# Kernel optimization log

Hardware: AMD Instinct MI355X
Metric: run time of the kernel (lower is better)

Reference implementation:

```python
import jax, jax.numpy as jnp
import numpy as np
import math

EMBED_DIM = 1024
NUM_HEADS = 16
HEAD_DIM = EMBED_DIM // NUM_HEADS
DIFFUSION_STEPS = 2
ALPHA = 0.05
DETACH_P = True


def setup_inputs() -> dict:
    key = jax.random.key(0)
    ks = jax.random.split(key, 9)
    B, N, D = 1, 2048, EMBED_DIM
    s = 1.0 / math.sqrt(D)
    inp = {
        "hidden_states": jax.random.normal(ks[0], (B, N, D), dtype=jnp.float32),
        # torch nn.Linear weight is [out,in]; we store [in,out] so y = x @ W + b
        "Wq": jax.random.normal(ks[1], (D, D), dtype=jnp.float32) * s,
        "bq": jnp.zeros((D,), dtype=jnp.float32),
        "Wk": jax.random.normal(ks[2], (D, D), dtype=jnp.float32) * s,
        "bk": jnp.zeros((D,), dtype=jnp.float32),
        "Wv": jax.random.normal(ks[3], (D, D), dtype=jnp.float32) * s,
        "bv": jnp.zeros((D,), dtype=jnp.float32),
        "Wo": jax.random.normal(ks[4], (D, D), dtype=jnp.float32) * s,
        "bo": jnp.zeros((D,), dtype=jnp.float32),
    }
    return inp


def reference(hidden_states, Wq, bq, Wk, bk, Wv, bv, Wo, bo):
    B, N, D = hidden_states.shape
    H, hd = NUM_HEADS, HEAD_DIM

    def split_heads(x):  # [B,N,D] -> [B,H,N,hd]
        return x.reshape(B, N, H, hd).transpose(0, 2, 1, 3)

    Q = split_heads(hidden_states @ Wq + bq)
    K = split_heads(hidden_states @ Wk + bk)
    V = split_heads(hidden_states @ Wv + bv)

    # standard QK^T attention probabilities
    scores = jnp.einsum('bhqd,bhkd->bhqk', Q, K) / math.sqrt(hd)
    p0 = jax.nn.softmax(scores, axis=-1)

    # transition matrix from keys (note: scaled by sqrt(embed_dim), not head_dim)
    sim = jnp.einsum('bhid,bhjd->bhij', K, K) / math.sqrt(D)
    P = jax.nn.softmax(sim, axis=-1)
    if DETACH_P:
        P = jax.lax.stop_gradient(P)

    # iterative diffusion: p <- (1-alpha)*p0 + alpha * p @ P
    p = p0
    for _ in range(DIFFUSION_STEPS):
        p = (1.0 - ALPHA) * p0 + ALPHA * jnp.einsum('bhqn,bhnm->bhqm', p, P)

    attn = jnp.einsum('bhqk,bhkd->bhqd', p, V)          # [B,H,N,hd]
    attn = attn.transpose(0, 2, 1, 3).reshape(B, N, H * hd)
    out = attn @ Wo + bo
    return out, p
```

## Files before the change

### kernel.cpp

```cpp
#include <hip/hip_runtime.h>

#define N_TOK 2048
#define DMODEL 1024
#define NHEAD 16
#define HDIM 64

typedef __attribute__((ext_vector_type(8))) __bf16 bf16x8;
typedef __attribute__((ext_vector_type(4))) float f32x4;
typedef __attribute__((ext_vector_type(4))) int i32x4;
typedef __attribute__((ext_vector_type(8))) int i32x8;

__device__ __forceinline__ float bf2f(unsigned short h) {
  return __uint_as_float(((unsigned int)h) << 16);
}
__device__ __forceinline__ unsigned short f2bf(float f) {
  unsigned int u = __float_as_uint(f);
  unsigned int r = (u + 0x7fffu + ((u >> 16) & 1u)) >> 16;
  return (unsigned short)r;
}
__device__ __forceinline__ unsigned int pack4_fp8(float a, float b, float c, float d) {
  int v = __builtin_amdgcn_cvt_pk_fp8_f32(a, b, 0, false);
  v = __builtin_amdgcn_cvt_pk_fp8_f32(c, d, v, true);
  return (unsigned int)v;
}
__device__ __forceinline__ int swz8(int k8, int row) {
  return k8 ^ ((row & 7) << 4);
}

__device__ __forceinline__ void async16(const void* g, void* l) {
  __builtin_amdgcn_global_load_lds((__attribute__((address_space(1))) void*)(g),
                                   (__attribute__((address_space(3))) void*)(l),
                                   16, 0, 0);
}

#define FP8_SCALE 256.0f
#define FP8_INV2  (1.0f / (256.0f * 256.0f))

struct GemmP {
  const unsigned short* A;
  const unsigned short* B;
  const unsigned short* Eb;
  const float* bias;
  float* Cf;
  unsigned short* Cb;
  long long sA, sB, sE, sCf, sCb;
  int lda, ldb, ldE, ldCf, ldCb;
  int M, N, K;
  float alpha, beta;
};

__global__ __launch_bounds__(256) void gemm_bt_kernel(GemmP g) {
  __shared__ __attribute__((aligned(16))) unsigned short As[128 * 32];
  __shared__ __attribute__((aligned(16))) unsigned short Bs[128 * 32];
  const int tid = threadIdx.x;
  const int lane = tid & 63;
  const int wv = tid >> 6;
  const int wr = wv >> 1, wc = wv & 1;
  const long long z = blockIdx.z;
  const unsigned short* A = g.A + z * g.sA;
  const unsigned short* B = g.B + z * g.sB;
  const int tm = blockIdx.y * 128;
  const int tn = blockIdx.x * 128;

  const int r0 = tid >> 2;
  const int r1 = (tid + 256) >> 2;
  const int kof = (tid & 3) * 8;
  int bn0 = tn + r0; if (bn0 > g.N - 1) bn0 = g.N - 1;
  int bn1 = tn + r1; if (bn1 > g.N - 1) bn1 = g.N - 1;

  const unsigned short* pa0 = A + (long long)(tm + r0) * g.lda + kof;
  const unsigned short* pa1 = A + (long long)(tm + r1) * g.lda + kof;
  const unsigned short* pb0 = B + (long long)bn0 * g.ldb + kof;
  const unsigned short* pb1 = B + (long long)bn1 * g.ldb + kof;

  unsigned short* la0 = &As[tid * 8];
  unsigned short* la1 = &As[(tid + 256) * 8];
  unsigned short* lb0 = &Bs[tid * 8];
  unsigned short* lb1 = &Bs[(tid + 256) * 8];

  const int aroff = (wr * 64 + (lane & 15)) * 32 + (lane >> 4) * 8;
  const int broff = (wc * 64 + (lane & 15)) * 32 + (lane >> 4) * 8;

  f32x4 acc[4][4] = {};

  for (int kk = 0; kk < g.K; kk += 32) {
    __syncthreads();
    async16(pa0 + kk, la0);
    async16(pa1 + kk, la1);
    async16(pb0 + kk, lb0);
    async16(pb1 + kk, lb1);
    __syncthreads();
    bf16x8 af[4], bfr[4];
#pragma unroll
    for (int i = 0; i < 4; i++)
      af[i] = *(const bf16x8*)&As[aroff + i * 16 * 32];
#pragma unroll
    for (int j = 0; j < 4; j++)
      bfr[j] = *(const bf16x8*)&Bs[broff + j * 16 * 32];
#pragma unroll
    for (int i = 0; i < 4; i++)
#pragma unroll
      for (int j = 0; j < 4; j++)
        acc[i][j] = __builtin_amdgcn_mfma_f32_16x16x32_bf16(af[i], bfr[j], acc[i][j], 0, 0, 0);
  }

  const unsigned short* Eb = g.Eb ? g.Eb + z * g.sE : nullptr;
  float* Cf = g.Cf ? g.Cf + z * g.sCf : nullptr;
  unsigned short* Cb = g.Cb ? g.Cb + z * g.sCb : nullptr;
  const int cbase = tn + wc * 64 + (lane & 15);
  const int rbase = tm + wr * 64 + (lane >> 4) * 4;
#pragma unroll
  for (int i = 0; i < 4; i++) {
#pragma unroll
    for (int j = 0; j < 4; j++) {
      int col = cbase + j * 16;
      if (col < g.N) {
        float bs = g.bias ? g.bias[col] : 0.f;
#pragma unroll
        for (int r = 0; r < 4; r++) {
          int row = rbase + i * 16 + r;
          float v = g.alpha * acc[i][j][r] + bs;
          if (Eb) v += g.beta * bf2f(Eb[(long long)row * g.ldE + col]);
          if (Cf) Cf[(long long)row * g.ldCf + col] = v;
          if (Cb) Cb[(long long)row * g.ldCb + col] = f2bf(v);
        }
      }
    }
  }
}

struct QKP {
  const unsigned short* A;
  const unsigned short* B;
  float* mx;
  float* rz;
  unsigned short* Pbf;
  unsigned char* P8;
  float scale;
  int colstats;
};

__global__ __launch_bounds__(256) void qk_stats_kernel(QKP g) {
  __shared__ __attribute__((aligned(16))) unsigned short Qs[128 * 64];
  __shared__ __attribute__((aligned(16))) unsigned short Ks[2][128 * 64];
  __shared__ float redA[2][128];
  __shared__ float redB[2][128];
  const int tid = threadIdx.x;
  const int lane = tid & 63;
  const int wv = tid >> 6;
  const int wr = wv >> 1, wc = wv & 1;
  const int z = blockIdx.y;
  const int tm = blockIdx.x * 128;
  const unsigned short* A = g.A + z * HDIM;
  const unsigned short* B = g.B + z * HDIM;

  int sr[4], so[4];
#pragma unroll
  for (int k = 0; k < 4; k++) {
    int c = tid + k * 256;
    int row = c >> 3;
    sr[k] = row;
    so[k] = ((c & 7) ^ (row & 7)) * 8;
  }
#pragma unroll
  for (int k = 0; k < 4; k++)
    async16(A + (long long)(tm + sr[k]) * DMODEL + so[k], (char*)Qs + tid * 16 + k * 4096);
#pragma unroll
  for (int k = 0; k < 4; k++)
    async16(B + (long long)sr[k] * DMODEL + so[k], (char*)Ks[0] + tid * 16 + k * 4096);
  asm volatile("s_waitcnt vmcnt(0)" ::: "memory");
  __builtin_amdgcn_s_barrier();

  const int fr = lane & 15;
  const int fg = lane >> 4;
  bf16x8 qf[4][2];
#pragma unroll
  for (int i = 0; i < 4; i++)
#pragma unroll
    for (int s = 0; s < 2; s++) {
      int r = wr * 64 + fr + i * 16;
      int gl = (fg + s * 4) ^ (r & 7);
      qf[i][s] = *(const bf16x8*)&Qs[r * 64 + gl * 8];
    }

  float m_[16], s_[16], mn_[16], t_[16];
#pragma unroll
  for (int q = 0; q < 16; q++) { m_[q] = -3.0e38f; s_[q] = 0.f; }

  int buf = 0;
  for (int kb = 0; kb < 16; kb++) {
    f32x4 acc[4][4] = {};
#pragma unroll
    for (int j = 0; j < 4; j++) {
      int r = wc * 64 + fr + j * 16;
#pragma unroll
      for (int s = 0; s < 2; s++) {
        int gl = (fg + s * 4) ^ (r & 7);
        bf16x8 bf = *(const bf16x8*)&Ks[buf][r * 64 + gl * 8];
#pragma unroll
        for (int i = 0; i < 4; i++)
          acc[i][j] = __builtin_amdgcn_mfma_f32_16x16x32_bf16(qf[i][s], bf, acc[i][j], 0, 0, 0);
      }
    }
    if (kb < 15) {
#pragma unroll
      for (int k = 0; k < 4; k++)
        async16(B + (long long)((kb + 1) * 128 + sr[k]) * DMODEL + so[k],
                (char*)Ks[buf ^ 1] + tid * 16 + k * 4096);
    }
#pragma unroll
    for (int i = 0; i < 4; i++)
#pragma unroll
      for (int r = 0; r < 4; r++) {
        float mm = fmaxf(fmaxf(acc[i][0][r], acc[i][1][r]),
                         fmaxf(acc[i][2][r], acc[i][3][r]));
        mn_[i * 4 + r] = mm * g.scale;
      }
#pragma unroll
    for (int q = 0; q < 16; q++) {
      float v = mn_[q];
      v = fmaxf(v, __shfl_xor(v, 1));
      v = fmaxf(v, __shfl_xor(v, 2));
      v = fmaxf(v, __shfl_xor(v, 4));
      v = fmaxf(v, __shfl_xor(v, 8));
      mn_[q] = v;
    }
    if (fr == 0) {
#pragma unroll
      for (int i = 0; i < 4; i++)
#pragma unroll
        for (int r = 0; r < 4; r++)
          redA[wc][wr * 64 + i * 16 + fg * 4 + r] = mn_[i * 4 + r];
    }
    __builtin_amdgcn_s_barrier();
#pragma unroll
    for (int i = 0; i < 4; i++)
#pragma unroll
      for (int r = 0; r < 4; r++) {
        int row = wr * 64 + i * 16 + fg * 4 + r;
        int q = i * 4 + r;
        float mn = fmaxf(m_[q], fmaxf(redA[0][row], redA[1][row]));
        float e0 = __expf(acc[i][0][r] * g.scale - mn);
        float e1 = __expf(acc[i][1][r] * g.scale - mn);
        float e2 = __expf(acc[i][2][r] * g.scale - mn);
        float e3 = __expf(acc[i][3][r] * g.scale - mn);
        t_[q] = (e0 + e1) + (e2 + e3);
        mn_[q] = mn;
      }
#pragma unroll
    for (int q = 0; q < 16; q++) {
      float v = t_[q];
      v += __shfl_xor(v, 1);
      v += __shfl_xor(v, 2);
      v += __shfl_xor(v, 4);
      v += __shfl_xor(v, 8);
      t_[q] = v;
    }
    if (fr == 0) {
#pragma unroll
      for (int i = 0; i < 4; i++)
#pragma unroll
        for (int r = 0; r < 4; r++)
          redB[wc][wr * 64 + i * 16 + fg * 4 + r] = t_[i * 4 + r];
    }
    __builtin_amdgcn_s_barrier();
#pragma unroll
    for (int i = 0; i < 4; i++)
#pragma unroll
      for (int r = 0; r < 4; r++) {
        int row = wr * 64 + i * 16 + fg * 4 + r;
        int q = i * 4 + r;
        float tt = redB[0][row] + redB[1][row];
        s_[q] = s_[q] * __expf(m_[q] - mn_[q]) + tt;
        m_[q] = mn_[q];
      }
    if (kb < 15) asm volatile("s_waitcnt vmcnt(0)" ::: "memory");
    __builtin_amdgcn_s_barrier();
    buf ^= 1;
  }

  if (fr == 0 && wc == 0) {
#pragma unroll
    for (int i = 0; i < 4; i++)
#pragma unroll
      for (int r = 0; r < 4; r++) {
        int row = wr * 64 + i * 16 + fg * 4 + r;
        int q = i * 4 + r;
        g.mx[(long long)z * N_TOK + tm + row] = m_[q];
        g.rz[(long long)z * N_TOK + tm + row] = 1.f / s_[q];
      }
  }
}

__global__ __launch_bounds__(256) void qk_emit_kernel(QKP g) {
  __shared__ __attribute__((aligned(16))) unsigned short Qs[128 * 64];
  __shared__ __attribute__((aligned(16))) unsigned short Ks[2][128 * 64];
  __shared__ __attribute__((aligned(16))) float Ps[128 * 128];
  const int tid = threadIdx.x;
  const int lane = tid & 63;
  const int wv = tid >> 6;
  const int wr = wv >> 1, wc = wv & 1;
  const int z = blockIdx.y;
  const int tm = blockIdx.x * 128;
  const unsigned short* A = g.A + z * HDIM;
  const unsigned short* B = g.B + z * HDIM;

  int sr[4], so[4];
#pragma unroll
  for (int k = 0; k < 4; k++) {
    int c = tid + k * 256;
    int row = c >> 3;
    sr[k] = row;
    so[k] = ((c & 7) ^ (row & 7)) * 8;
  }
#pragma unroll
  for (int k = 0; k < 4; k++)
    async16(A + (long long)(tm + sr[k]) * DMODEL + so[k], (char*)Qs + tid * 16 + k * 4096);
#pragma unroll
  for (int k = 0; k < 4; k++)
    async16(B + (long long)sr[k] * DMODEL + so[k], (char*)Ks[0] + tid * 16 + k * 4096);
  asm volatile("s_waitcnt vmcnt(0)" ::: "memory");
  __builtin_amdgcn_s_barrier();

  const int fr = lane & 15;
  const int fg = lane >> 4;
  bf16x8 qf[4][2];
#pragma unroll
  for (int i = 0; i < 4; i++)
#pragma unroll
    for (int s = 0; s < 2; s++) {
      int r = wr * 64 + fr + i * 16;
      int gl = (fg + s * 4) ^ (r & 7);
      qf[i][s] = *(const bf16x8*)&Qs[r * 64 + gl * 8];
    }

  const int rr = tid >> 5;
  const int c4 = (tid & 31) * 4;
  const long long zn = (long long)z * N_TOK;
  float mr_[16], rr_[16];
  if (!g.colstats) {
#pragma unroll
    for (int p = 0; p < 16; p++) {
      mr_[p] = g.mx[zn + tm + p * 8 + rr];
      rr_[p] = g.rz[zn + tm + p * 8 + rr];
    }
  }

  int buf = 0;
  for (int kb = 0; kb < 16; kb++) {
    f32x4 acc[4][4] = {};
#pragma unroll
    for (int j = 0; j < 4; j++) {
      int r = wc * 64 + fr + j * 16;
#pragma unroll
      for (int s = 0; s < 2; s++) {
        int gl = (fg + s * 4) ^ (r & 7);
        bf16x8 bf = *(const bf16x8*)&Ks[buf][r * 64 + gl * 8];
#pragma unroll
        for (int i = 0; i < 4; i++)
          acc[i][j] = __builtin_amdgcn_mfma_f32_16x16x32_bf16(qf[i][s], bf, acc[i][j], 0, 0, 0);
      }
    }
#pragma unroll
    for (int i = 0; i < 4; i++)
#pragma unroll
      for (int j = 0; j < 4; j++)
#pragma unroll
        for (int r = 0; r < 4; r++)
          Ps[(wr * 64 + i * 16 + fg * 4 + r) * 128 + wc * 64 + fr + j * 16] =
              acc[i][j][r] * g.scale;
    __builtin_amdgcn_s_barrier();
    if (kb < 15) {
#pragma unroll
      for (int k = 0; k < 4; k++)
        async16(B + (long long)((kb + 1) * 128 + sr[k]) * DMODEL + so[k],
                (char*)Ks[buf ^ 1] + tid * 16 + k * 4096);
    }
    const int ct = kb * 128;
    float ma[4], ra[4];
    if (g.colstats) {
      float4 m4 = *(const float4*)&g.mx[zn + ct + c4];
      float4 r4 = *(const float4*)&g.rz[zn + ct + c4];
      ma[0] = m4.x; ma[1] = m4.y; ma[2] = m4.z; ma[3] = m4.w;
      ra[0] = r4.x; ra[1] = r4.y; ra[2] = r4.z; ra[3] = r4.w;
    }
#pragma unroll
    for (int p = 0; p < 16; p++) {
      int row = p * 8 + rr;
      f32x4 v = *(const f32x4*)&Ps[row * 128 + c4];
      float pr[4];
      if (g.colstats) {
        pr[0] = __expf(v.x - ma[0]) * ra[0];
        pr[1] = __expf(v.y - ma[1]) * ra[1];
        pr[2] = __expf(v.z - ma[2]) * ra[2];
        pr[3] = __expf(v.w - ma[3]) * ra[3];
      } else {
        pr[0] = __expf(v.x - mr_[p]) * rr_[p];
        pr[1] = __expf(v.y - mr_[p]) * rr_[p];
        pr[2] = __expf(v.z - mr_[p]) * rr_[p];
        pr[3] = __expf(v.w - mr_[p]) * rr_[p];
      }
      long long prow = (zn + tm + row) * N_TOK;
      if (g.Pbf) {
        uint2 ob;
        ob.x = (unsigned)f2bf(pr[0]) | ((unsigned)f2bf(pr[1]) << 16);
        ob.y = (unsigned)f2bf(pr[2]) | ((unsigned)f2bf(pr[3]) << 16);
        *(uint2*)&g.Pbf[prow + ct + c4] = ob;
      }
      unsigned o8 = pack4_fp8(pr[0] * FP8_SCALE, pr[1] * FP8_SCALE,
                              pr[2] * FP8_SCALE, pr[3] * FP8_SCALE);
      *(unsigned*)&g.P8[prow + ((ct + c4) ^ ((row & 7) << 4))] = o8;
    }
    if (kb < 15) asm volatile("s_waitcnt vmcnt(0)" ::: "memory");
    __builtin_amdgcn_s_barrier();
    buf ^= 1;
  }
}

struct Gemm8P {
  const unsigned char* A;
  const unsigned char* B;
  const unsigned short* Eb;
  float* Cf;
  unsigned short* Cb;
  long long sA, sB, sE, sCf, sCb;
  int lda, ldb, ldE, ldCf, ldCb;
  int K;
  float alpha, beta;
};

__global__ __launch_bounds__(256) void gemm_fp8_kernel(Gemm8P g) {
  __shared__ __attribute__((aligned(16))) unsigned char smem[65536];
  unsigned char* As0 = smem;
  unsigned char* Bs0 = smem + 32768;
  float* Cs = (float*)smem;
  const int tid = threadIdx.x;
  const int lane = tid & 63;
  const int wv = tid >> 6;
  const int wr = wv >> 1, wc = wv & 1;

  const unsigned int nx = gridDim.x, ny = gridDim.y;
  unsigned int orig = (blockIdx.z * ny + blockIdx.y) * nx + blockIdx.x;
  unsigned int nwg = nx * ny * gridDim.z;
  unsigned int wg = (orig & 7) * (nwg >> 3) + (orig >> 3);
  const int bx = wg % nx;
  unsigned int t1 = wg / nx;
  const int by = t1 % ny;
  const int bz = t1 / ny;

  const long long z = bz;
  const unsigned char* A = g.A + z * g.sA;
  const unsigned char* B = g.B + z * g.sB;
  const int tm = by * 128;
  const int tn = bx * 128;

  const int rs = tid >> 3;
  const int ks = (tid & 7) * 16;
  const unsigned char* pa0 = A + (long long)(tm + rs) * g.lda + ks;
  const unsigned char* pb0 = B + (long long)(tn + rs) * g.ldb + ks;
  const long long sa32 = 32LL * g.lda;
  const long long sb32 = 32LL * g.ldb;

  const int sw = (lane & 7) << 4;
  const int kg = (lane >> 4) * 32;
  const int klo = kg ^ sw;
  const int khi = (kg + 16) ^ sw;
  const int aoff0 = (wr * 64 + (lane & 15)) * 128;
  const int boff0 = (wc * 64 + (lane & 15)) * 128;

  f32x4 acc[4][4] = {};

  auto STAGE = [&](int buf, int kk) {
    unsigned char* la = As0 + buf * 16384 + tid * 16;
    unsigned char* lb = Bs0 + buf * 16384 + tid * 16;
    async16(pa0 + kk, la);
    async16(pa0 + sa32 + kk, la + 4096);
    async16(pa0 + 2 * sa32 + kk, la + 8192);
    async16(pa0 + 3 * sa32 + kk, la + 12288);
    async16(pb0 + kk, lb);
    async16(pb0 + sb32 + kk, lb + 4096);
    async16(pb0 + 2 * sb32 + kk, lb + 8192);
    async16(pb0 + 3 * sb32 + kk, lb + 12288);
  };

  auto COMPUTE = [&](int buf) {
    const unsigned char* ab = As0 + buf * 16384;
    const unsigned char* bb = Bs0 + buf * 16384;
    i32x8 a8[4], b8[4];
#pragma unroll
    for (int i = 0; i < 4; i++) {
      i32x4 lo = *(const i32x4*)(ab + aoff0 + i * 16 * 128 + klo);
      i32x4 hi = *(const i32x4*)(ab + aoff0 + i * 16 * 128 + khi);
      a8[i] = __builtin_shufflevector(lo, hi, 0, 1, 2, 3, 4, 5, 6, 7);
    }
#pragma unroll
    for (int j = 0; j < 4; j++) {
      i32x4 lo = *(const i32x4*)(bb + boff0 + j * 16 * 128 + klo);
      i32x4 hi = *(const i32x4*)(bb + boff0 + j * 16 * 128 + khi);
      b8[j] = __builtin_shufflevector(lo, hi, 0, 1, 2, 3, 4, 5, 6, 7);
    }
#pragma unroll
    for (int i = 0; i < 4; i++)
#pragma unroll
      for (int j = 0; j < 4; j++)
        acc[i][j] = __builtin_amdgcn_mfma_scale_f32_16x16x128_f8f6f4(
            a8[i], b8[j], acc[i][j], 0, 0, 0, 0x7f7f7f7f, 0, 0x7f7f7f7f);
  };

  const int NT = g.K >> 7;
  STAGE(0, 0);
  int cur = 0;
  for (int t = 0; t < NT - 1; ++t) {
    STAGE(cur ^ 1, (t + 1) << 7);
    asm volatile("s_waitcnt vmcnt(8)" ::: "memory");
    __builtin_amdgcn_s_barrier();
    __builtin_amdgcn_sched_barrier(0);
    COMPUTE(cur);
    __builtin_amdgcn_sched_barrier(0);
    __builtin_amdgcn_s_barrier();
    cur ^= 1;
  }
  asm volatile("s_waitcnt vmcnt(0)" ::: "memory");
  __builtin_amdgcn_s_barrier();
  __builtin_amdgcn_sched_barrier(0);
  COMPUTE(cur);

  __syncthreads();
  const int lrow0 = wr * 64 + (lane >> 4) * 4;
  const int lcol0 = wc * 64 + (lane & 15);
#pragma unroll
  for (int i = 0; i < 4; i++)
#pragma unroll
    for (int j = 0; j < 4; j++)
#pragma unroll
      for (int r = 0; r < 4; r++)
        Cs[(lrow0 + i * 16 + r) * 128 + lcol0 + j * 16] = acc[i][j][r];
  __syncthreads();

  const unsigned short* Eb = g.Eb + z * g.sE;
  float* Cf = g.Cf + z * g.sCf;
  unsigned short* Cb = g.Cb + z * g.sCb;
  const int rr = tid >> 5;
  const int c4 = (tid & 31) * 4;
#pragma unroll
  for (int p = 0; p < 16; p++) {
    int row = p * 8 + rr;
    f32x4 v = *(const f32x4*)&Cs[row * 128 + c4];
    long long gr = (long long)(tm + row);
    uint2 e = *(const uint2*)&Eb[gr * g.ldE + tn + c4];
    f32x4 o;
    o.x = g.alpha * v.x + g.beta * bf2f((unsigned short)(e.x & 0xffff));
    o.y = g.alpha * v.y + g.beta * bf2f((unsigned short)(e.x >> 16));
    o.z = g.alpha * v.z + g.beta * bf2f((unsigned short)(e.y & 0xffff));
    o.w = g.alpha * v.w + g.beta * bf2f((unsigned short)(e.y >> 16));
    *(f32x4*)&Cf[gr * g.ldCf + tn + c4] = o;
    uint2 ob;
    ob.x = (unsigned)f2bf(o.x) | ((unsigned)f2bf(o.y) << 16);
    ob.y = (unsigned)f2bf(o.z) | ((unsigned)f2bf(o.w) << 16);
    *(uint2*)&Cb[gr * g.ldCb + tn + c4] = ob;
  }
}

struct AttnP {
  const unsigned short* A;
  const unsigned short* B;
  float* Part;
  long long sA, sB;
  int lda, ldb, G;
};

__global__ __launch_bounds__(256) void attn_part_kernel(AttnP g) {
  __shared__ __attribute__((aligned(16))) unsigned short As[128 * 32];
  __shared__ __attribute__((aligned(16))) unsigned short Bs[64 * 32];
  const int tid = threadIdx.x;
  const int lane = tid & 63;
  const int w = tid >> 6;
  const int z = blockIdx.y;
  const int kz = blockIdx.z;
  const unsigned short* A = g.A + (long long)z * g.sA;
  const unsigned short* B = g.B + (long long)z * g.sB;
  const int tm = blockIdx.x * 128;
  const int k0 = kz * 512;

  const int rA0 = tid >> 2;
  const int rA1 = 64 + (tid >> 2);
  const int kof = (tid & 3) * 8;
  const unsigned short* pa0 = A + (long long)(tm + rA0) * g.lda + k0 + kof;
  const unsigned short* pa1 = A + (long long)(tm + rA1) * g.lda + k0 + kof;
  const unsigned short* pb0 = B + (long long)(tid >> 2) * g.ldb + k0 + kof;
  unsigned short* la0 = &As[tid * 8];
  unsigned short* la1 = &As[(tid + 256) * 8];
  unsigned short* lb0 = &Bs[tid * 8];

  const int aoff = (w * 32 + (lane & 15)) * 32 + (lane >> 4) * 8;
  const int boff = (lane & 15) * 32 + (lane >> 4) * 8;

  f32x4 acc[2][4] = {};

  for (int kk = 0; kk < 512; kk += 32) {
    __syncthreads();
    async16(pa0 + kk, la0);
    async16(pa1 + kk, la1);
    async16(pb0 + kk, lb0);
    __syncthreads();
    bf16x8 af[2], bfr[4];
#pragma unroll
    for (int i = 0; i < 2; i++)
      af[i] = *(const bf16x8*)&As[aoff + i * 16 * 32];
#pragma unroll
    for (int j = 0; j < 4; j++)
      bfr[j] = *(const bf16x8*)&Bs[boff + j * 16 * 32];
#pragma unroll
    for (int i = 0; i < 2; i++)
#pragma unroll
      for (int j = 0; j < 4; j++)
        acc[i][j] = __builtin_amdgcn_mfma_f32_16x16x32_bf16(af[i], bfr[j], acc[i][j], 0, 0, 0);
  }

  float* P = g.Part + ((long long)(kz * g.G + z) * N_TOK + tm) * 64;
#pragma unroll
  for (int i = 0; i < 2; i++) {
#pragma unroll
    for (int j = 0; j < 4; j++) {
      int col = (lane & 15) + j * 16;
#pragma unroll
      for (int r = 0; r < 4; r++) {
        int row = w * 32 + i * 16 + (lane >> 4) * 4 + r;
        P[(long long)row * 64 + col] = acc[i][j][r];
      }
    }
  }
}

__global__ __launch_bounds__(256) void attn_reduce_kernel(const float* Part, unsigned short* ATT,
                                                          int G, int h0) {
  int idx = blockIdx.x * 256 + threadIdx.x;
  int f = idx * 4;
  int z = f / (N_TOK * 64);
  int rem = f % (N_TOK * 64);
  int row = rem >> 6;
  int col = rem & 63;
  long long stride = (long long)G * N_TOK * 64;
  const float* p0 = Part + ((long long)z * N_TOK + row) * 64 + col;
  float4 s = *(const float4*)p0;
  float4 a = *(const float4*)(p0 + stride);
  float4 b = *(const float4*)(p0 + 2 * stride);
  float4 c = *(const float4*)(p0 + 3 * stride);
  s.x += a.x + b.x + c.x; s.y += a.y + b.y + c.y;
  s.z += a.z + b.z + c.z; s.w += a.w + b.w + c.w;
  uint2 o;
  o.x = (unsigned)f2bf(s.x) | ((unsigned)f2bf(s.y) << 16);
  o.y = (unsigned)f2bf(s.z) | ((unsigned)f2bf(s.w) << 16);
  *(uint2*)&ATT[(long long)row * DMODEL + (h0 + z) * 64 + col] = o;
}


__global__ __launch_bounds__(256) void cast_f32_bf16_kernel(const float* x, unsigned short* y) {
  int i = blockIdx.x * 256 + threadIdx.x;
  const float4* src = (const float4*)x;
  float4 a = src[i * 2], b = src[i * 2 + 1];
  uint4 o;
  o.x = (unsigned)f2bf(a.x) | ((unsigned)f2bf(a.y) << 16);
  o.y = (unsigned)f2bf(a.z) | ((unsigned)f2bf(a.w) << 16);
  o.z = (unsigned)f2bf(b.x) | ((unsigned)f2bf(b.y) << 16);
  o.w = (unsigned)f2bf(b.z) | ((unsigned)f2bf(b.w) << 16);
  ((uint4*)y)[i] = o;
}

__global__ __launch_bounds__(256) void transpose_w_kernel(const float* in, unsigned short* out,
                                                          int rows, int cols) {
  __shared__ float t[32][33];
  int c = blockIdx.x * 32 + threadIdx.x;
  int r0 = blockIdx.y * 32;
#pragma unroll
  for (int j = 0; j < 32; j += 8)
    t[threadIdx.y + j][threadIdx.x] = in[(long long)(r0 + threadIdx.y + j) * cols + c];
  __syncthreads();
  int r = r0 + threadIdx.x;
#pragma unroll
  for (int j = 0; j < 32; j += 8)
    out[(long long)(blockIdx.x * 32 + threadIdx.y + j) * rows + r] =
        f2bf(t[threadIdx.x][threadIdx.y + j]);
}

__global__ __launch_bounds__(256) void transpose_bf_kernel(const unsigned short* in,
                                                           unsigned short* out,
                                                           int rows, int cols) {
  __shared__ unsigned short t[32][34];
  int c = blockIdx.x * 32 + threadIdx.x;
  int r0 = blockIdx.y * 32;
#pragma unroll
  for (int j = 0; j < 32; j += 8)
    t[threadIdx.y + j][threadIdx.x] = in[(long long)(r0 + threadIdx.y + j) * cols + c];
  __syncthreads();
  int r = r0 + threadIdx.x;
#pragma unroll
  for (int j = 0; j < 32; j += 8)
    out[(long long)(blockIdx.x * 32 + threadIdx.y + j) * rows + r] = t[threadIdx.x][threadIdx.y + j];
}


extern "C" void kernel_launch(void* const* d_in, const int* in_sizes, int n_in,
                              void* d_out, int out_size, void* d_ws, size_t ws_size,
                              hipStream_t stream) {
  const float* hs = (const float*)d_in[0];
  const float* Wq = (const float*)d_in[1];
  const float* bq = (const float*)d_in[2];
  const float* Wk = (const float*)d_in[3];
  const float* bk = (const float*)d_in[4];
  const float* Wv = (const float*)d_in[5];
  const float* bv = (const float*)d_in[6];
  const float* Wo = (const float*)d_in[7];
  const float* bo = (const float*)d_in[8];
  float* out = (float*)d_out;
  float* outp = out + (size_t)N_TOK * DMODEL;

  char* base = (char*)d_ws;
  size_t off = 0;
  auto alloc = [&](size_t bytes) -> void* {
    void* p = base + off;
    off += (bytes + 255) & ~(size_t)255;
    return p;
  };
  const size_t ND2 = (size_t)N_TOK * DMODEL * 2;
  unsigned short* Xbf = (unsigned short*)alloc(ND2);
  unsigned short* Qbf = (unsigned short*)alloc(ND2);
  unsigned short* Kbf = (unsigned short*)alloc(ND2);
  unsigned short* Vbf = (unsigned short*)alloc(ND2);
  unsigned short* Vt  = (unsigned short*)alloc(ND2);
  unsigned short* ATT = (unsigned short*)alloc(ND2);
  unsigned short* WT  = (unsigned short*)alloc((size_t)DMODEL * DMODEL * 2);
  float* mx = (float*)alloc((size_t)NHEAD * N_TOK * 4);
  float* rz = (float*)alloc((size_t)NHEAD * N_TOK * 4);
  float* mxq = (float*)alloc((size_t)NHEAD * N_TOK * 4);
  float* rzq = (float*)alloc((size_t)NHEAD * N_TOK * 4);
  float* Part = (float*)alloc((size_t)4 * NHEAD * N_TOK * 64 * 4);
  size_t fixed = off;

  const size_t SZ = (size_t)N_TOK * N_TOK;
  int G = 16;
  while (G > 1 && fixed + (size_t)G * SZ * 8 > ws_size) G >>= 1;
  float* SB           = (float*)alloc((size_t)G * SZ * 4);
  unsigned short* P0  = (unsigned short*)alloc((size_t)G * SZ * 2);
  unsigned char* P0q  = (unsigned char*)alloc((size_t)G * SZ);
  unsigned char* PT   = (unsigned char*)alloc((size_t)G * SZ);
  unsigned short* PB   = (unsigned short*)SB + G * SZ;

  auto gemm = [&](const GemmP& p, int nt, int mt, int batch) {
    gemm_bt_kernel<<<dim3(nt, mt, batch), 256, 0, stream>>>(p);
  };

  cast_f32_bf16_kernel<<<(N_TOK * DMODEL / 8) / 256, 256, 0, stream>>>(hs, Xbf);

  auto proj = [&](const float* W, const float* bias, unsigned short* dst) {
    transpose_w_kernel<<<dim3(32, 32), dim3(32, 8), 0, stream>>>(W, WT, DMODEL, DMODEL);
    GemmP p = {};
    p.A = Xbf; p.lda = DMODEL;
    p.B = WT;  p.ldb = DMODEL;
    p.bias = bias;
    p.Cb = dst; p.ldCb = DMODEL;
    p.M = N_TOK; p.N = DMODEL; p.K = DMODEL;
    p.alpha = 1.f;
    gemm(p, DMODEL / 128, N_TOK / 128, 1);
  };
  proj(Wq, bq, Qbf);
  proj(Wk, bk, Kbf);
  proj(Wv, bv, Vbf);
  transpose_bf_kernel<<<dim3(DMODEL / 32, N_TOK / 32), dim3(32, 8), 0, stream>>>(Vbf, Vt, N_TOK, DMODEL);

  const float sc_hd = 0.125f;
  const float sc_d  = 0.03125f;
  const float alpha = 0.05f;

  int ngroups = NHEAD / G;
  for (int gi = 0; gi < ngroups; gi++) {
    int h0 = gi * G;

    QKP qp = {};
    qp.A = Qbf + h0 * HDIM; qp.B = Kbf + h0 * HDIM;
    qp.mx = mxq; qp.rz = rzq; qp.scale = sc_hd; qp.colstats = 0;
    qk_stats_kernel<<<dim3(16, G), 256, 0, stream>>>(qp);
    qp.Pbf = P0; qp.P8 = P0q;
    qk_emit_kernel<<<dim3(16, G), 256, 0, stream>>>(qp);

    QKP sp = {};
    sp.A = Kbf + h0 * HDIM; sp.B = Kbf + h0 * HDIM;
    sp.mx = mx; sp.rz = rz; sp.scale = sc_d; sp.colstats = 1;
    qk_stats_kernel<<<dim3(16, G), 256, 0, stream>>>(sp);
    sp.Pbf = nullptr; sp.P8 = PT;
    qk_emit_kernel<<<dim3(16, G), 256, 0, stream>>>(sp);

    Gemm8P g8 = {};
    g8.A = P0q; g8.sA = (long long)SZ; g8.lda = N_TOK;
    g8.B = PT;  g8.sB = (long long)SZ; g8.ldb = N_TOK;
    g8.Eb = P0; g8.sE = (long long)SZ; g8.ldE = N_TOK;
    g8.Cf = outp + (size_t)h0 * SZ; g8.sCf = (long long)SZ; g8.ldCf = N_TOK;
    g8.Cb = PB; g8.sCb = (long long)SZ; g8.ldCb = N_TOK;
    g8.K = N_TOK;
    g8.alpha = alpha * FP8_INV2;
    g8.beta = 1.f - alpha;
    gemm_fp8_kernel<<<dim3(16, 16, G), 256, 0, stream>>>(g8);

    AttnP pa = {};
    pa.A = PB; pa.sA = (long long)SZ; pa.lda = N_TOK;
    pa.B = Vt + (size_t)h0 * HDIM * N_TOK; pa.sB = (long long)HDIM * N_TOK; pa.ldb = N_TOK;
    pa.Part = Part; pa.G = G;
    attn_part_kernel<<<dim3(16, G, 4), 256, 0, stream>>>(pa);
    attn_reduce_kernel<<<G * 128, 256, 0, stream>>>(Part, ATT, G, h0);
  }

  transpose_w_kernel<<<dim3(32, 32), dim3(32, 8), 0, stream>>>(Wo, WT, DMODEL, DMODEL);
  GemmP po = {};
  po.A = ATT; po.lda = DMODEL;
  po.B = WT;  po.ldb = DMODEL;
  po.bias = bo;
  po.Cf = out; po.ldCf = DMODEL;
  po.M = N_TOK; po.N = DMODEL; po.K = DMODEL;
  po.alpha = 1.f;
  gemm(po, DMODEL / 128, N_TOK / 128, 1);
}
```

Baseline: 963.6 us.

## Double-buffer GEMM loads, stage epilogue through LDS, batch QKV projections

The bf16 GEMM and attention partial kernels now prefetch the next K tile into a second LDS buffer while computing the current one, using vmcnt waits and barriers instead of two syncthreads per step. Both epilogues now write through shared memory so global stores are coalesced float4 rows. The three Q/K/V weight transposes and projection GEMMs are merged into one batched launch, with biases copied into a contiguous buffer. This cuts launch count and load latency at the cost of 64KB LDS per GEMM block, which may lower occupancy.

```diff
diff --git a/kernel.cpp b/kernel.cpp
--- a/kernel.cpp
+++ b/kernel.cpp
@@ -22,9 +22,6 @@
   int v = __builtin_amdgcn_cvt_pk_fp8_f32(a, b, 0, false);
   v = __builtin_amdgcn_cvt_pk_fp8_f32(c, d, v, true);
   return (unsigned int)v;
-}
-__device__ __forceinline__ int swz8(int k8, int row) {
-  return k8 ^ ((row & 7) << 4);
 }
 
 __device__ __forceinline__ void async16(const void* g, void* l) {
@@ -43,15 +40,17 @@
   const float* bias;
   float* Cf;
   unsigned short* Cb;
-  long long sA, sB, sE, sCf, sCb;
+  long long sA, sB, sE, sCf, sCb, sBias;
   int lda, ldb, ldE, ldCf, ldCb;
   int M, N, K;
   float alpha, beta;
 };
 
 __global__ __launch_bounds__(256) void gemm_bt_kernel(GemmP g) {
-  __shared__ __attribute__((aligned(16))) unsigned short As[128 * 32];
-  __shared__ __attribute__((aligned(16))) unsigned short Bs[128 * 32];
+  __shared__ __attribute__((aligned(16))) unsigned char smem[65536];
+  unsigned short* As0 = (unsigned short*)smem;
+  unsigned short* Bs0 = (unsigned short*)(smem + 32768);
+  float* Cs = (float*)smem;
   const int tid = threadIdx.x;
   const int lane = tid & 63;
   const int wv = tid >> 6;
@@ -73,57 +72,99 @@
   const unsigned short* pb0 = B + (long long)bn0 * g.ldb + kof;
   const unsigned short* pb1 = B + (long long)bn1 * g.ldb + kof;
 
-  unsigned short* la0 = &As[tid * 8];
-  unsigned short* la1 = &As[(tid + 256) * 8];
-  unsigned short* lb0 = &Bs[tid * 8];
-  unsigned short* lb1 = &Bs[(tid + 256) * 8];
-
   const int aroff = (wr * 64 + (lane & 15)) * 32 + (lane >> 4) * 8;
   const int broff = (wc * 64 + (lane & 15)) * 32 + (lane >> 4) * 8;
 
   f32x4 acc[4][4] = {};
 
-  for (int kk = 0; kk < g.K; kk += 32) {
-    __syncthreads();
-    async16(pa0 + kk, la0);
-    async16(pa1 + kk, la1);
-    async16(pb0 + kk, lb0);
-    async16(pb1 + kk, lb1);
-    __syncthreads();
+  auto STAGE = [&](int buf, int kk) {
+    unsigned short* la = As0 + buf * 4096 + tid * 8;
+    unsigned short* lb = Bs0 + buf * 4096 + tid * 8;
+    async16(pa0 + kk, la);
+    async16(pa1 + kk, la + 2048);
+    async16(pb0 + kk, lb);
+    async16(pb1 + kk, lb + 2048);
+  };
+  auto COMPUTE = [&](int buf) {
+    const unsigned short* ab = As0 + buf * 4096;
+    const unsigned short* bb = Bs0 + buf * 4096;
     bf16x8 af[4], bfr[4];
 #pragma unroll
     for (int i = 0; i < 4; i++)
-      af[i] = *(const bf16x8*)&As[aroff + i * 16 * 32];
+      af[i] = *(const bf16x8*)&ab[aroff + i * 512];
 #pragma unroll
     for (int j = 0; j < 4; j++)
-      bfr[j] = *(const bf16x8*)&Bs[broff + j * 16 * 32];
+      bfr[j] = *(const bf16x8*)&bb[broff + j * 512];
 #pragma unroll
     for (int i = 0; i < 4; i++)
 #pragma unroll
       for (int j = 0; j < 4; j++)
         acc[i][j] = __builtin_amdgcn_mfma_f32_16x16x32_bf16(af[i], bfr[j], acc[i][j], 0, 0, 0);
-  }
+  };
+
+  const int NT = g.K >> 5;
+  STAGE(0, 0);
+  int cur = 0;
+  for (int t = 0; t < NT - 1; ++t) {
+    STAGE(cur ^ 1, (t + 1) << 5);
+    asm volatile("s_waitcnt vmcnt(4)" ::: "memory");
+    __builtin_amdgcn_s_barrier();
+    __builtin_amdgcn_sched_barrier(0);
+    COMPUTE(cur);
+    __builtin_amdgcn_sched_barrier(0);
+    __builtin_amdgcn_s_barrier();
+    cur ^= 1;
+  }
+  asm volatile("s_waitcnt vmcnt(0)" ::: "memory");
+  __builtin_amdgcn_s_barrier();
+  __builtin_amdgcn_sched_barrier(0);
+  COMPUTE(cur);
+
+  __syncthreads();
+  const int lrow0 = wr * 64 + (lane >> 4) * 4;
+  const int lcol0 = wc * 64 + (lane & 15);
+#pragma unroll
+  for (int i = 0; i < 4; i++)
+#pragma unroll
+    for (int j = 0; j < 4; j++)
+#pragma unroll
+      for (int r = 0; r < 4; r++)
+        Cs[(lrow0 + i * 16 + r) * 128 + lcol0 + j * 16] = acc[i][j][r];
+  __syncthreads();
 
   const unsigned short* Eb = g.Eb ? g.Eb + z * g.sE : nullptr;
   float* Cf = g.Cf ? g.Cf + z * g.sCf : nullptr;
   unsigned short* Cb = g.Cb ? g.Cb + z * g.sCb : nullptr;
-  const int cbase = tn + wc * 64 + (lane & 15);
-  const int rbase = tm + wr * 64 + (lane >> 4) * 4;
-#pragma unroll
-  for (int i = 0; i < 4; i++) {
-#pragma unroll
-    for (int j = 0; j < 4; j++) {
-      int col = cbase + j * 16;
-      if (col < g.N) {
-        float bs = g.bias ? g.bias[col] : 0.f;
-#pragma unroll
-        for (int r = 0; r < 4; r++) {
-          int row = rbase + i * 16 + r;
-          float v = g.alpha * acc[i][j][r] + bs;
-          if (Eb) v += g.beta * bf2f(Eb[(long long)row * g.ldE + col]);
-          if (Cf) Cf[(long long)row * g.ldCf + col] = v;
-          if (Cb) Cb[(long long)row * g.ldCb + col] = f2bf(v);
-        }
+  const float* bias = g.bias ? g.bias + z * g.sBias : nullptr;
+  const int rr = tid >> 5;
+  const int c4 = (tid & 31) * 4;
+  const int coln = tn + c4;
+  float4 b4 = {0.f, 0.f, 0.f, 0.f};
+  if (bias && coln < g.N) b4 = *(const float4*)&bias[coln];
+  if (coln < g.N) {
+#pragma unroll
+    for (int p = 0; p < 16; p++) {
+      int row = p * 8 + rr;
+      f32x4 v = *(const f32x4*)&Cs[row * 128 + c4];
+      long long gr = (long long)(tm + row);
+      f32x4 o;
+      o.x = g.alpha * v.x + b4.x;
+      o.y = g.alpha * v.y + b4.y;
+      o.z = g.alpha * v.z + b4.z;
+      o.w = g.alpha * v.w + b4.w;
+      if (Eb) {
+        uint2 e = *(const uint2*)&Eb[gr * g.ldE + coln];
+        o.x += g.beta * bf2f((unsigned short)(e.x & 0xffff));
+        o.y += g.beta * bf2f((unsigned short)(e.x >> 16));
+        o.z += g.beta * bf2f((unsigned short)(e.y & 0xffff));
+        o.w += g.beta * bf2f((unsigned short)(e.y >> 16));
+      }
+      if (Cf) *(f32x4*)&Cf[gr * g.ldCf + coln] = o;
+      if (Cb) {
+        uint2 ob;
+        ob.x = (unsigned)f2bf(o.x) | ((unsigned)f2bf(o.y) << 16);
+        ob.y = (unsigned)f2bf(o.z) | ((unsigned)f2bf(o.w) << 16);
+        *(uint2*)&Cb[gr * g.ldCb + coln] = ob;
       }
     }
   }
@@ -570,8 +611,10 @@
 };
 
 __global__ __launch_bounds__(256) void attn_part_kernel(AttnP g) {
-  __shared__ __attribute__((aligned(16))) unsigned short As[128 * 32];
-  __shared__ __attribute__((aligned(16))) unsigned short Bs[64 * 32];
+  __shared__ __attribute__((aligned(16))) unsigned char smem[32768];
+  unsigned short* As0 = (unsigned short*)smem;
+  unsigned short* Bs0 = (unsigned short*)(smem + 16384);
+  float* Cs = (float*)smem;
   const int tid = threadIdx.x;
   const int lane = tid & 63;
   const int w = tid >> 6;
@@ -588,47 +631,71 @@
   const unsigned short* pa0 = A + (long long)(tm + rA0) * g.lda + k0 + kof;
   const unsigned short* pa1 = A + (long long)(tm + rA1) * g.lda + k0 + kof;
   const unsigned short* pb0 = B + (long long)(tid >> 2) * g.ldb + k0 + kof;
-  unsigned short* la0 = &As[tid * 8];
-  unsigned short* la1 = &As[(tid + 256) * 8];
-  unsigned short* lb0 = &Bs[tid * 8];
 
   const int aoff = (w * 32 + (lane & 15)) * 32 + (lane >> 4) * 8;
   const int boff = (lane & 15) * 32 + (lane >> 4) * 8;
 
   f32x4 acc[2][4] = {};
 
-  for (int kk = 0; kk < 512; kk += 32) {
-    __syncthreads();
-    async16(pa0 + kk, la0);
-    async16(pa1 + kk, la1);
-    async16(pb0 + kk, lb0);
-    __syncthreads();
+  auto STAGE = [&](int buf, int kk) {
+    unsigned short* la = As0 + buf * 4096 + tid * 8;
+    unsigned short* lb = Bs0 + buf * 2048 + tid * 8;
+    async16(pa0 + kk, la);
+    async16(pa1 + kk, la + 2048);
+    async16(pb0 + kk, lb);
+  };
+  auto COMPUTE = [&](int buf) {
+    const unsigned short* ab = As0 + buf * 4096;
+    const unsigned short* bb = Bs0 + buf * 2048;
     bf16x8 af[2], bfr[4];
 #pragma unroll
     for (int i = 0; i < 2; i++)
-      af[i] = *(const bf16x8*)&As[aoff + i * 16 * 32];
+      af[i] = *(const bf16x8*)&ab[aoff + i * 512];
 #pragma unroll
     for (int j = 0; j < 4; j++)
-      bfr[j] = *(const bf16x8*)&Bs[boff + j * 16 * 32];
+      bfr[j] = *(const bf16x8*)&bb[boff + j * 512];
 #pragma unroll
     for (int i = 0; i < 2; i++)
 #pragma unroll
       for (int j = 0; j < 4; j++)
         acc[i][j] = __builtin_amdgcn_mfma_f32_16x16x32_bf16(af[i], bfr[j], acc[i][j], 0, 0, 0);
-  }
+  };
+
+  STAGE(0, 0);
+  int cur = 0;
+  for (int t = 0; t < 15; ++t) {
+    STAGE(cur ^ 1, (t + 1) << 5);
+    asm volatile("s_waitcnt vmcnt(3)" ::: "memory");
+    __builtin_amdgcn_s_barrier();
+    __builtin_amdgcn_sched_barrier(0);
+    COMPUTE(cur);
+    __builtin_amdgcn_sched_barrier(0);
+    __builtin_amdgcn_s_barrier();
+    cur ^= 1;
+  }
+  asm volatile("s_waitcnt vmcnt(0)" ::: "memory");
+  __builtin_amdgcn_s_barrier();
+  __builtin_amdgcn_sched_barrier(0);
+  COMPUTE(cur);
+
+  __syncthreads();
+#pragma unroll
+  for (int i = 0; i < 2; i++)
+#pragma unroll
+    for (int j = 0; j < 4; j++)
+#pragma unroll
+      for (int r = 0; r < 4; r++)
+        Cs[(w * 32 + i * 16 + (lane >> 4) * 4 + r) * 64 + (lane & 15) + j * 16] = acc[i][j][r];
+  __syncthreads();
 
   float* P = g.Part + ((long long)(kz * g.G + z) * N_TOK + tm) * 64;
-#pragma unroll
-  for (int i = 0; i < 2; i++) {
-#pragma unroll
-    for (int j = 0; j < 4; j++) {
-      int col = (lane & 15) + j * 16;
-#pragma unroll
-      for (int r = 0; r < 4; r++) {
-        int row = w * 32 + i * 16 + (lane >> 4) * 4 + r;
-        P[(long long)row * 64 + col] = acc[i][j][r];
-      }
-    }
+  const int rr = tid >> 4;
+  const int c4 = (tid & 15) * 4;
+#pragma unroll
+  for (int p = 0; p < 8; p++) {
+    int row = p * 16 + rr;
+    f32x4 v = *(const f32x4*)&Cs[row * 64 + c4];
+    *(f32x4*)&P[(long long)row * 64 + c4] = v;
   }
 }
 
@@ -683,6 +750,30 @@
         f2bf(t[threadIdx.x][threadIdx.y + j]);
 }
 
+struct TW3 {
+  const float* W0;
+  const float* W1;
+  const float* W2;
+  unsigned short* out;
+};
+
+__global__ __launch_bounds__(256) void transpose_w3_kernel(TW3 p, int rows, int cols) {
+  __shared__ float t[32][33];
+  const float* in = (blockIdx.z == 0) ? p.W0 : (blockIdx.z == 1) ? p.W1 : p.W2;
+  unsigned short* out = p.out + (size_t)blockIdx.z * rows * cols;
+  int c = blockIdx.x * 32 + threadIdx.x;
+  int r0 = blockIdx.y * 32;
+#pragma unroll
+  for (int j = 0; j < 32; j += 8)
+    t[threadIdx.y + j][threadIdx.x] = in[(long long)(r0 + threadIdx.y + j) * cols + c];
+  __syncthreads();
+  int r = r0 + threadIdx.x;
+#pragma unroll
+  for (int j = 0; j < 32; j += 8)
+    out[(long long)(blockIdx.x * 32 + threadIdx.y + j) * rows + r] =
+        f2bf(t[threadIdx.x][threadIdx.y + j]);
+}
+
 __global__ __launch_bounds__(256) void transpose_bf_kernel(const unsigned short* in,
                                                            unsigned short* out,
                                                            int rows, int cols) {
@@ -730,6 +821,8 @@
   unsigned short* Vt  = (unsigned short*)alloc(ND2);
   unsigned short* ATT = (unsigned short*)alloc(ND2);
   unsigned short* WT  = (unsigned short*)alloc((size_t)DMODEL * DMODEL * 2);
+  unsigned short* WT3 = (unsigned short*)alloc((size_t)3 * DMODEL * DMODEL * 2);
+  float* bias3 = (float*)alloc((size_t)3 * DMODEL * 4);
   float* mx = (float*)alloc((size_t)NHEAD * N_TOK * 4);
   float* rz = (float*)alloc((size_t)NHEAD * N_TOK * 4);
   float* mxq = (float*)alloc((size_t)NHEAD * N_TOK * 4);
@@ -746,26 +839,23 @@
   unsigned char* PT   = (unsigned char*)alloc((size_t)G * SZ);
   unsigned short* PB   = (unsigned short*)SB + G * SZ;
 
-  auto gemm = [&](const GemmP& p, int nt, int mt, int batch) {
-    gemm_bt_kernel<<<dim3(nt, mt, batch), 256, 0, stream>>>(p);
-  };
-
   cast_f32_bf16_kernel<<<(N_TOK * DMODEL / 8) / 256, 256, 0, stream>>>(hs, Xbf);
 
-  auto proj = [&](const float* W, const float* bias, unsigned short* dst) {
-    transpose_w_kernel<<<dim3(32, 32), dim3(32, 8), 0, stream>>>(W, WT, DMODEL, DMODEL);
+  TW3 tw = {Wq, Wk, Wv, WT3};
+  transpose_w3_kernel<<<dim3(32, 32, 3), dim3(32, 8), 0, stream>>>(tw, DMODEL, DMODEL);
+  hipMemcpyAsync(bias3, bq, DMODEL * 4, hipMemcpyDeviceToDevice, stream);
+  hipMemcpyAsync(bias3 + DMODEL, bk, DMODEL * 4, hipMemcpyDeviceToDevice, stream);
+  hipMemcpyAsync(bias3 + 2 * DMODEL, bv, DMODEL * 4, hipMemcpyDeviceToDevice, stream);
+  {
     GemmP p = {};
-    p.A = Xbf; p.lda = DMODEL;
-    p.B = WT;  p.ldb = DMODEL;
-    p.bias = bias;
-    p.Cb = dst; p.ldCb = DMODEL;
+    p.A = Xbf; p.lda = DMODEL; p.sA = 0;
+    p.B = WT3; p.ldb = DMODEL; p.sB = (long long)DMODEL * DMODEL;
+    p.bias = bias3; p.sBias = DMODEL;
+    p.Cb = Qbf; p.ldCb = DMODEL; p.sCb = (long long)N_TOK * DMODEL;
     p.M = N_TOK; p.N = DMODEL; p.K = DMODEL;
     p.alpha = 1.f;
-    gemm(p, DMODEL / 128, N_TOK / 128, 1);
-  };
-  proj(Wq, bq, Qbf);
-  proj(Wk, bk, Kbf);
-  proj(Wv, bv, Vbf);
+    gemm_bt_kernel<<<dim3(DMODEL / 128, N_TOK / 128, 3), 256, 0, stream>>>(p);
+  }
   transpose_bf_kernel<<<dim3(DMODEL / 32, N_TOK / 32), dim3(32, 8), 0, stream>>>(Vbf, Vt, N_TOK, DMODEL);
 
   const float sc_hd = 0.125f;
@@ -817,5 +907,5 @@
   po.Cf = out; po.ldCf = DMODEL;
   po.M = N_TOK; po.N = DMODEL; po.K = DMODEL;
   po.alpha = 1.f;
-  gemm(po, DMODEL / 128, N_TOK / 128, 1);
-}
+  gemm_bt_kernel<<<dim3(DMODEL / 128, N_TOK / 128, 1), 256, 0, stream>>>(po);
+}
```

Measured after the change: 886.8 us. -8.0%, faster.
